# Kernel optimization log

Measured on AMD Instinct MI355X. Metric: run time of the kernel, lower is better.

The kernel has to match this reference:

```python
import jax, jax.numpy as jnp
import numpy as np

N, D_IN, HID, NH = 16384, 2048, 2048, 16
HD = HID // NH  # head_size = 128


def setup_inputs() -> dict:
    key = jax.random.key(0)
    ks = jax.random.split(key, 8)
    s = 1.0 / np.sqrt(D_IN)
    return {
        "protein": jax.random.normal(ks[0], (N, D_IN), jnp.float32),
        "drug": jax.random.normal(ks[1], (N, D_IN), jnp.float32),
        "mask_prot": jnp.ones((N,), bool),
        "mask_drug": jnp.ones((N,), bool),
        "Wq_p": jax.random.uniform(ks[2], (D_IN, HID), jnp.float32, -s, s),
        "Wk_p": jax.random.uniform(ks[3], (D_IN, HID), jnp.float32, -s, s),
        "Wv_p": jax.random.uniform(ks[4], (D_IN, HID), jnp.float32, -s, s),
        "Wq_d": jax.random.uniform(ks[5], (D_IN, HID), jnp.float32, -s, s),
        "Wk_d": jax.random.uniform(ks[6], (D_IN, HID), jnp.float32, -s, s),
        "Wv_d": jax.random.uniform(ks[7], (D_IN, HID), jnp.float32, -s, s),
    }


def _heads(x):
    # [N, L, HID] -> [N, L, NH, HD]
    return x.reshape(x.shape[0], x.shape[1], NH, HD)


def _alpha_logits(logits, mask_row, mask_col, inf=1e6):
    # logits: [N, L1, L2, H]; masks: [N, L1], [N, L2] (broadcast over heads)
    mask_pair = mask_row[:, :, None, None] & mask_col[:, None, :, None]
    logits = jnp.where(mask_pair, logits, logits - inf)
    alpha = jax.nn.softmax(logits, axis=2)
    alpha = jnp.where(mask_row[:, :, None, None], alpha, jnp.zeros_like(alpha))
    return alpha


def reference(protein, drug, mask_prot, mask_drug, Wq_p, Wk_p, Wv_p, Wq_d, Wk_d, Wv_d):
    p = protein[:, None, :]  # [N, 1, D_IN]
    d = drug[:, None, :]
    # forward() overwrites the masks with all-ones of shape [N, L=1]
    m_p = jnp.ones(p.shape[:-1], bool)
    m_d = jnp.ones(d.shape[:-1], bool)

    qp = _heads(jnp.einsum('bld,dh->blh', p, Wq_p))  # [N,1,NH,HD]
    kp = _heads(jnp.einsum('bld,dh->blh', p, Wk_p))
    vp = _heads(jnp.einsum('bld,dh->blh', p, Wv_p))
    qd = _heads(jnp.einsum('bld,dh->blh', d, Wq_d))
    kd = _heads(jnp.einsum('bld,dh->blh', d, Wk_d))
    vd = _heads(jnp.einsum('bld,dh->blh', d, Wv_d))

    logits_pp = jnp.einsum('blhd,bkhd->blkh', qp, kp)
    logits_pd = jnp.einsum('blhd,bkhd->blkh', qp, kd)
    logits_dp = jnp.einsum('blhd,bkhd->blkh', qd, kp)
    logits_dd = jnp.einsum('blhd,bkhd->blkh', qd, kd)

    a_pp = _alpha_logits(logits_pp, m_p, m_p)
    a_pd = _alpha_logits(logits_pd, m_p, m_d)
    a_dp = _alpha_logits(logits_dp, m_d, m_p)
    a_dd = _alpha_logits(logits_dd, m_d, m_d)

    def agg(alpha, v):
        out = jnp.einsum('blkh,bkhd->blhd', alpha, v)
        return out.reshape(out.shape[0], out.shape[1], HID)

    prot_embedding = (agg(a_pp, vp) + agg(a_pd, vd)) / 2  # [N,1,HID]
    drug_embedding = (agg(a_dp, vp) + agg(a_dd, vd)) / 2

    # agg_mode == 'cls'
    prot_embed = prot_embedding[:, 0]
    drug_embed = drug_embedding[:, 0]
    return jnp.concatenate([prot_embed, drug_embed], axis=1)  # [N, 2*HID]
```

## Files before the change

kernel.cpp:

```cpp
#include <hip/hip_runtime.h>
#include <stdint.h>


typedef __attribute__((ext_vector_type(8))) short short8;
typedef __attribute__((ext_vector_type(4))) float float4v;
typedef __attribute__((ext_vector_type(2))) unsigned int uint2v;

typedef const __attribute__((address_space(1))) unsigned int* gp_t;
typedef __attribute__((address_space(3))) unsigned int* lp_t;

#define M_DIM 16384
#define N_DIM 2048
#define K_DIM 4096
#define OUT_LD 4096

static __device__ __forceinline__ unsigned int pack_bf16x2(float x, float y) {
  union { float f; unsigned int u; } a, b;
  a.f = x; b.f = y;
  unsigned int ua = a.u + 0x8000u;
  unsigned int ub = b.u + 0x8000u;
  return __builtin_amdgcn_perm(ub, ua, 0x07060302u);
}

static __device__ __forceinline__ unsigned short f2bf(float x) {
  union { float f; unsigned int u; } a; a.f = x;
  return (unsigned short)((a.u + 0x8000u) >> 16);
}

__global__ __launch_bounds__(256)
void prep_wt(const float* __restrict__ Wp, const float* __restrict__ Wd,
             unsigned short* __restrict__ Wt) {
  __shared__ float tile[32][33];
  const int k0 = blockIdx.x * 32;
  const int n0 = blockIdx.y * 32;
  const int tx = threadIdx.x;
  const int ty = threadIdx.y;
  const float* W = (k0 < 2048) ? Wp : Wd;
  const int kk0 = (k0 < 2048) ? k0 : k0 - 2048;
#pragma unroll
  for (int i = 0; i < 4; ++i) {
    int r = ty * 4 + i;
    tile[r][tx] = W[(size_t)(kk0 + r) * 2048 + n0 + tx];
  }
  __syncthreads();
#pragma unroll
  for (int i = 0; i < 4; ++i) {
    int r = ty * 4 + i;
    Wt[(size_t)(n0 + r) * (size_t)K_DIM + k0 + tx] = f2bf(tile[tx][r]);
  }
}

__global__ __launch_bounds__(256)
void cast_a(const float* __restrict__ P, const float* __restrict__ Dg,
            unsigned int* __restrict__ Abf) {
  int idx = blockIdx.x * 256 + threadIdx.x;
  int row = idx >> 10;
  int j = (idx & 1023) << 2;
  const float* src = (j < 2048) ? (P + (size_t)row * 2048 + j)
                                : (Dg + (size_t)row * 2048 + (j - 2048));
  float4v v = *(const float4v*)src;
  uint2v o;
  o.x = pack_bf16x2(v.x, v.y);
  o.y = pack_bf16x2(v.z, v.w);
  *(uint2v*)(Abf + (size_t)row * 2048 + (j >> 1)) = o;
}


#define VMW(N) asm volatile("s_waitcnt vmcnt(" #N ")" ::: "memory")
#define LGW0() asm volatile("s_waitcnt lgkmcnt(0)" ::: "memory")
#define BAR() __builtin_amdgcn_s_barrier()

#define LOAD_A(Ac, QM)                                                      \
  _Pragma("unroll") for (int i = 0; i < 4; ++i) {                           \
    af[i][0] = *(const short8*)&(Ac)[aoff + ((QM)*4 + i) * 1024 + c0];      \
    af[i][1] = *(const short8*)&(Ac)[aoff + ((QM)*4 + i) * 1024 + c1];      \
  }

#define LOAD_B2(dst, Bc, QN)                                                \
  _Pragma("unroll") for (int j = 0; j < 2; ++j) {                           \
    dst[j][0] = *(const short8*)&(Bc)[boff + ((QN)*2 + j) * 1024 + c0];     \
    dst[j][1] = *(const short8*)&(Bc)[boff + ((QN)*2 + j) * 1024 + c1];     \
  }

#define MFMA_Q(bset, QM, QN)                                                \
  _Pragma("unroll") for (int i = 0; i < 4; ++i)                             \
  _Pragma("unroll") for (int j = 0; j < 2; ++j) {                           \
    acc[(QM)*4 + i][(QN)*2 + j] = __builtin_amdgcn_mfma_f32_16x16x32_bf16(  \
        af[i][0], bset[j][0], acc[(QM)*4 + i][(QN)*2 + j], 0, 0, 0);        \
    acc[(QM)*4 + i][(QN)*2 + j] = __builtin_amdgcn_mfma_f32_16x16x32_bf16(  \
        af[i][1], bset[j][1], acc[(QM)*4 + i][(QN)*2 + j], 0, 0, 0);        \
  }

__global__ __launch_bounds__(512, 2)
void gemm8(const unsigned short* __restrict__ Abf,
           const unsigned short* __restrict__ Wt,
           float* __restrict__ out) {
  __shared__ unsigned short As[2][256 * 64];
  __shared__ unsigned short Bs[2][256 * 64];

  const int t = threadIdx.x;
  const int w = t >> 6, l = t & 63;
  const int wm = w >> 2, wn = w & 3;
  const int lr = l & 15, q16 = l >> 4, xr = lr & 7;

  const int bx = blockIdx.x;
  const int logical = (bx & 7) * 64 + (bx >> 3);
  const int tn = logical & 7, tm = logical >> 3;
  const int m0 = tm << 8, n0 = tn << 8;

  const int srow = t >> 3;
  const int sk = (((t & 7) ^ (srow & 7)) << 3);
  const int brr = srow & 31;
  const int bsel = t >> 8;

  auto stage_a = [&](int buf, int k0, int h) {
#pragma unroll
    for (int sub = 0; sub < 2; ++sub) {
      const int row = m0 + sub * 128 + h * 64 + srow;
      const unsigned short* g = Abf + (size_t)row * K_DIM + (k0 + sk);
      const int ldsrow0 = sub * 128 + h * 64 + (w << 3);
      __builtin_amdgcn_global_load_lds((gp_t)(const void*)g,
                                       (lp_t)&As[buf][ldsrow0 * 64], 16, 0, 0);
    }
  };
  auto stage_b = [&](int buf, int k0, int nh) {
#pragma unroll
    for (int sub = 0; sub < 2; ++sub) {
      const int wnr = sub * 2 + bsel;
      const int ncol = n0 + wnr * 64 + nh * 32 + brr;
      const unsigned short* g = Wt + (size_t)ncol * K_DIM + (k0 + sk);
      const int ldsrow0 = wnr * 64 + nh * 32 + ((w & 3) << 3);
      __builtin_amdgcn_global_load_lds((gp_t)(const void*)g,
                                       (lp_t)&Bs[buf][ldsrow0 * 64], 16, 0, 0);
    }
  };

  float4v acc[8][4];
#pragma unroll
  for (int i = 0; i < 8; ++i)
#pragma unroll
    for (int j = 0; j < 4; ++j)
      acc[i][j] = (float4v){0.f, 0.f, 0.f, 0.f};

  const int aoff = (wm * 128 + lr) * 64;
  const int boff = (wn * 64 + lr) * 64;
  const int c0 = (q16 ^ xr) << 3;
  const int c1 = ((4 + q16) ^ xr) << 3;

  stage_a(0, 0, 0);
  stage_b(0, 0, 0);
  stage_b(0, 0, 1);
  stage_a(0, 0, 1);
  stage_a(1, 64, 0);
  stage_b(1, 64, 0);
  stage_b(1, 64, 1);
  stage_a(1, 64, 1);
  VMW(8);
  BAR();

  for (int tt = 0; tt < 62; ++tt) {
    const int buf = tt & 1;
    unsigned short* Ac = &As[buf][0];
    unsigned short* Bc = &Bs[buf][0];
    const int k2 = tt * 64 + 128;
    short8 af[4][2];
    short8 b0r[2][2];
    short8 b1r[2][2];

    LOAD_A(Ac, 0)
    LOAD_B2(b0r, Bc, 0)
    BAR(); LGW0();
    __builtin_amdgcn_s_setprio(1);
    MFMA_Q(b0r, 0, 0)
    __builtin_amdgcn_s_setprio(0);
    BAR();

    LOAD_B2(b1r, Bc, 1)
    stage_a(buf, k2, 0);
    stage_b(buf, k2, 0);
    BAR(); LGW0();
    __builtin_amdgcn_s_setprio(1);
    MFMA_Q(b1r, 0, 1)
    __builtin_amdgcn_s_setprio(0);
    BAR();

    LOAD_A(Ac, 1)
    stage_b(buf, k2, 1);
    BAR(); LGW0();
    __builtin_amdgcn_s_setprio(1);
    MFMA_Q(b1r, 1, 1)
    __builtin_amdgcn_s_setprio(0);
    BAR();

    stage_a(buf, k2, 1);
    BAR();
    __builtin_amdgcn_s_setprio(1);
    MFMA_Q(b0r, 1, 0)
    __builtin_amdgcn_s_setprio(0);
    VMW(8);
    BAR();
  }

  VMW(0);
  BAR();
#pragma unroll
  for (int e = 0; e < 2; ++e) {
    unsigned short* Ac = &As[e][0];
    unsigned short* Bc = &Bs[e][0];
    short8 af[4][2];
    short8 b0r[2][2];
    short8 b1r[2][2];
    __builtin_amdgcn_s_setprio(1);
    LOAD_A(Ac, 0)
    LOAD_B2(b0r, Bc, 0)
    MFMA_Q(b0r, 0, 0)
    LOAD_B2(b1r, Bc, 1)
    MFMA_Q(b1r, 0, 1)
    LOAD_A(Ac, 1)
    MFMA_Q(b1r, 1, 1)
    MFMA_Q(b0r, 1, 0)
    __builtin_amdgcn_s_setprio(0);
  }

  const int rbase = m0 + wm * 128 + q16 * 4;
  const int cbase = n0 + wn * 64 + lr;
#pragma unroll
  for (int f = 0; f < 8; ++f)
#pragma unroll
    for (int j = 0; j < 4; ++j) {
      const int row = rbase + f * 16;
      const int col = cbase + j * 16;
#pragma unroll
      for (int r = 0; r < 4; ++r) {
        float v = acc[f][j][r] * 0.5f;
        size_t o = (size_t)(row + r) * (size_t)OUT_LD + col;
        out[o] = v;
        out[o + N_DIM] = v;
      }
    }
}

__global__ __launch_bounds__(256)
void gemm_k(const float* __restrict__ Ap, const float* __restrict__ Ad,
            const unsigned short* __restrict__ Wt,
            float* __restrict__ out) {
  __shared__ unsigned short As[128 * 64];
  __shared__ unsigned short Bsm[128 * 64];

  const int t = threadIdx.x;
  const int bx = blockIdx.x;
  const int tn = bx & 15, tm = bx >> 4;
  const int m0 = tm << 7, n0 = tn << 7;
  const int w = t >> 6, l = t & 63;
  const int wmm = w & 1, wnn = w >> 1;
  const int lr = l & 15, q = l >> 4;

  const int rB = t >> 3;
  const int kB = (t & 7) * 8;

  float4v acc[4][4];
#pragma unroll
  for (int i = 0; i < 4; ++i)
#pragma unroll
    for (int j = 0; j < 4; ++j)
      acc[i][j] = (float4v){0.f, 0.f, 0.f, 0.f};

  for (int k0 = 0; k0 < K_DIM; k0 += 64) {
#pragma unroll
    for (int i = 0; i < 4; ++i) {
      const unsigned short* g =
          Wt + (size_t)(n0 + i * 32 + rB) * (size_t)K_DIM + (k0 + kB);
      __builtin_amdgcn_global_load_lds((gp_t)(const void*)g,
                                       (lp_t)&Bsm[i * 2048 + w * 512], 16, 0, 0);
    }
    {
      const float* base;
      int kk;
      if (k0 < 2048) { base = Ap; kk = k0; } else { base = Ad; kk = k0 - 2048; }
      const int rA = t >> 4;
      const int cA = (t & 15) * 4;
#pragma unroll
      for (int i = 0; i < 8; ++i) {
        int m = i * 16 + rA;
        float4v v = *(const float4v*)(base + (size_t)(m0 + m) * 2048 + kk + cA);
        uint2v o;
        o.x = pack_bf16x2(v.x, v.y);
        o.y = pack_bf16x2(v.z, v.w);
        *(uint2v*)&As[m * 64 + cA] = o;
      }
    }
    __syncthreads();

#pragma unroll
    for (int ks = 0; ks < 2; ++ks) {
      short8 a2[4], b2[4];
#pragma unroll
      for (int i = 0; i < 4; ++i) {
        a2[i] = *(const short8*)&As[(wmm * 64 + i * 16 + lr) * 64 + ks * 32 + q * 8];
        b2[i] = *(const short8*)&Bsm[(wnn * 64 + i * 16 + lr) * 64 + ks * 32 + q * 8];
      }
#pragma unroll
      for (int i = 0; i < 4; ++i)
#pragma unroll
        for (int j = 0; j < 4; ++j)
          acc[i][j] = __builtin_amdgcn_mfma_f32_16x16x32_bf16(a2[i], b2[j],
                                                              acc[i][j], 0, 0, 0);
    }
    __syncthreads();
  }

#pragma unroll
  for (int i = 0; i < 4; ++i) {
    const int r0 = m0 + wmm * 64 + i * 16 + q * 4;
#pragma unroll
    for (int j = 0; j < 4; ++j) {
      const int c = n0 + wnn * 64 + j * 16 + lr;
#pragma unroll
      for (int r = 0; r < 4; ++r) {
        float v = acc[i][j][r] * 0.5f;
        size_t o = (size_t)(r0 + r) * (size_t)OUT_LD + c;
        out[o] = v;
        out[o + 2048] = v;
      }
    }
  }
}

__global__ __launch_bounds__(256)
void gemm_fallback(const float* __restrict__ P, const float* __restrict__ Dg,
                   const float* __restrict__ Wp, const float* __restrict__ Wd,
                   float* __restrict__ out) {
  __shared__ float Asf[64][17];
  __shared__ float Bsf[16][65];
  const int bx = blockIdx.x;
  const int by = blockIdx.y;
  const int t = threadIdx.x;
  const int tc = t & 15, trw = t >> 4;
  const int m0 = by * 64, n0 = bx * 64;
  float accf[4][4] = {};
  for (int k0 = 0; k0 < 4096; k0 += 16) {
    const float* Asrc = (k0 < 2048) ? P : Dg;
    const float* Bsrc = (k0 < 2048) ? Wp : Wd;
    const int kk = k0 & 2047;
#pragma unroll
    for (int i = 0; i < 4; ++i) {
      int r = i * 16 + trw;
      Asf[r][tc] = Asrc[(size_t)(m0 + r) * 2048 + kk + tc];
    }
#pragma unroll
    for (int i = 0; i < 4; ++i) {
      int r = i * 4 + (t >> 6);
      int c = t & 63;
      Bsf[r][c] = Bsrc[(size_t)(kk + r) * 2048 + n0 + c];
    }
    __syncthreads();
#pragma unroll
    for (int k2 = 0; k2 < 16; ++k2) {
      float a[4], b[4];
#pragma unroll
      for (int i = 0; i < 4; ++i) a[i] = Asf[trw * 4 + i][k2];
#pragma unroll
      for (int j = 0; j < 4; ++j) b[j] = Bsf[k2][tc * 4 + j];
#pragma unroll
      for (int i = 0; i < 4; ++i)
#pragma unroll
        for (int j = 0; j < 4; ++j) accf[i][j] += a[i] * b[j];
    }
    __syncthreads();
  }
#pragma unroll
  for (int i = 0; i < 4; ++i)
#pragma unroll
    for (int j = 0; j < 4; ++j) {
      float v = accf[i][j] * 0.5f;
      size_t o = (size_t)(m0 + trw * 4 + i) * 4096 + n0 + tc * 4 + j;
      out[o] = v;
      out[o + 2048] = v;
    }
}

extern "C" void kernel_launch(void* const* d_in, const int* in_sizes, int n_in,
                              void* d_out, int out_size, void* d_ws, size_t ws_size,
                              hipStream_t stream) {
  const float* protein = (const float*)d_in[0];
  const float* drug    = (const float*)d_in[1];
  const float* Wv_p    = (const float*)d_in[6];
  const float* Wv_d    = (const float*)d_in[9];
  float* out = (float*)d_out;

  const size_t wt_bytes = (size_t)N_DIM * K_DIM * sizeof(unsigned short);
  const size_t a_bytes  = (size_t)M_DIM * K_DIM * sizeof(unsigned short);

  if (ws_size >= wt_bytes) {
    unsigned short* Wt = (unsigned short*)d_ws;
    prep_wt<<<dim3(128, 64), dim3(32, 8), 0, stream>>>(Wv_p, Wv_d, Wt);
    if (ws_size >= wt_bytes + a_bytes) {
      unsigned int* Abf = (unsigned int*)((char*)d_ws + wt_bytes);
      cast_a<<<65536, 256, 0, stream>>>(protein, drug, Abf);
      gemm8<<<512, 512, 0, stream>>>((const unsigned short*)Abf, Wt, out);
    } else {
      gemm_k<<<2048, 256, 0, stream>>>(protein, drug, Wt, out);
    }
  } else {
    gemm_fallback<<<dim3(32, 256), 256, 0, stream>>>(protein, drug, Wv_p, Wv_d, out);
  }
}
```

Measured before the change: 825.8 us.

## Reschedule GEMM pipeline stages and relax launch bounds to one block per CU

```diff
diff --git a/kernel.cpp b/kernel.cpp
--- a/kernel.cpp
+++ b/kernel.cpp
@@ -65,10 +65,12 @@
   *(uint2v*)(Abf + (size_t)row * 2048 + (j >> 1)) = o;
 }
 
-
 #define VMW(N) asm volatile("s_waitcnt vmcnt(" #N ")" ::: "memory")
 #define LGW0() asm volatile("s_waitcnt lgkmcnt(0)" ::: "memory")
+#define LGW8() asm volatile("s_waitcnt lgkmcnt(8)" ::: "memory")
 #define BAR() __builtin_amdgcn_s_barrier()
+#define SP1 __builtin_amdgcn_s_setprio(1);
+#define SP0 __builtin_amdgcn_s_setprio(0);
 
 #define LOAD_A(Ac, QM)                                                      \
   _Pragma("unroll") for (int i = 0; i < 4; ++i) {                           \
@@ -91,7 +93,7 @@
         af[i][1], bset[j][1], acc[(QM)*4 + i][(QN)*2 + j], 0, 0, 0);        \
   }
 
-__global__ __launch_bounds__(512, 2)
+__global__ __launch_bounds__(512, 1)
 void gemm8(const unsigned short* __restrict__ Abf,
            const unsigned short* __restrict__ Wt,
            float* __restrict__ out) {
@@ -154,63 +156,77 @@
   stage_a(1, 64, 0);
   stage_b(1, 64, 0);
   stage_b(1, 64, 1);
-  stage_a(1, 64, 1);
-  VMW(8);
+  VMW(6);
   BAR();
 
+  short8 af[4][2];
+  short8 b0r[2][2];
+  short8 b1r[2][2];
   for (int tt = 0; tt < 62; ++tt) {
     const int buf = tt & 1;
     unsigned short* Ac = &As[buf][0];
     unsigned short* Bc = &Bs[buf][0];
+    const int k1 = tt * 64 + 64;
     const int k2 = tt * 64 + 128;
-    short8 af[4][2];
-    short8 b0r[2][2];
-    short8 b1r[2][2];
 
     LOAD_A(Ac, 0)
     LOAD_B2(b0r, Bc, 0)
-    BAR(); LGW0();
-    __builtin_amdgcn_s_setprio(1);
-    MFMA_Q(b0r, 0, 0)
-    __builtin_amdgcn_s_setprio(0);
+    stage_a(buf ^ 1, k1, 1);
+    LGW8();
+    BAR(); LGW0();
+    SP1 MFMA_Q(b0r, 0, 0) SP0
     BAR();
 
     LOAD_B2(b1r, Bc, 1)
     stage_a(buf, k2, 0);
+    BAR(); LGW0();
+    SP1 MFMA_Q(b1r, 0, 1) SP0
+    BAR();
+
+    LOAD_A(Ac, 1)
     stage_b(buf, k2, 0);
     BAR(); LGW0();
-    __builtin_amdgcn_s_setprio(1);
-    MFMA_Q(b1r, 0, 1)
-    __builtin_amdgcn_s_setprio(0);
+    SP1 MFMA_Q(b1r, 1, 1) SP0
+    BAR();
+
+    stage_b(buf, k2, 1);
+    BAR();
+    SP1 MFMA_Q(b0r, 1, 0) SP0
+    VMW(6);
+    BAR();
+  }
+
+  {
+    unsigned short* Ac = &As[0][0];
+    unsigned short* Bc = &Bs[0][0];
+
+    LOAD_A(Ac, 0)
+    LOAD_B2(b0r, Bc, 0)
+    stage_a(1, 4032, 1);
+    LGW8();
+    BAR(); LGW0();
+    SP1 MFMA_Q(b0r, 0, 0) SP0
+    BAR();
+
+    LOAD_B2(b1r, Bc, 1)
+    BAR(); LGW0();
+    SP1 MFMA_Q(b1r, 0, 1) SP0
     BAR();
 
     LOAD_A(Ac, 1)
-    stage_b(buf, k2, 1);
-    BAR(); LGW0();
-    __builtin_amdgcn_s_setprio(1);
-    MFMA_Q(b1r, 1, 1)
-    __builtin_amdgcn_s_setprio(0);
-    BAR();
-
-    stage_a(buf, k2, 1);
-    BAR();
-    __builtin_amdgcn_s_setprio(1);
-    MFMA_Q(b0r, 1, 0)
-    __builtin_amdgcn_s_setprio(0);
-    VMW(8);
-    BAR();
-  }
-
-  VMW(0);
-  BAR();
-#pragma unroll
-  for (int e = 0; e < 2; ++e) {
-    unsigned short* Ac = &As[e][0];
-    unsigned short* Bc = &Bs[e][0];
-    short8 af[4][2];
-    short8 b0r[2][2];
-    short8 b1r[2][2];
-    __builtin_amdgcn_s_setprio(1);
+    BAR(); LGW0();
+    SP1 MFMA_Q(b1r, 1, 1) SP0
+    BAR();
+
+    SP1 MFMA_Q(b0r, 1, 0) SP0
+    VMW(0);
+    BAR();
+  }
+
+  {
+    unsigned short* Ac = &As[1][0];
+    unsigned short* Bc = &Bs[1][0];
+    SP1
     LOAD_A(Ac, 0)
     LOAD_B2(b0r, Bc, 0)
     MFMA_Q(b0r, 0, 0)
@@ -219,7 +235,7 @@
     LOAD_A(Ac, 1)
     MFMA_Q(b1r, 1, 1)
     MFMA_Q(b0r, 1, 0)
-    __builtin_amdgcn_s_setprio(0);
+    SP0
   }
 
   const int rbase = m0 + wm * 128 + q16 * 4;
```

Measured after the change: 787.4 us. 1.05x faster.
